# Performance work log

Measured on AMD Instinct MI355X. Metric: run time of the kernel, lower is better.

Reference implementation:

```python
import jax, jax.numpy as jnp
import numpy as np

BN_EPS = 1e-5


def _gin_layer(h, src, dst, w1, b1, w2, b2, gamma, beta):
    n = h.shape[0]
    # GINConv, eps=0: MLP(x + sum_{j->i} x_j); messages gathered at src, scattered to dst
    agg = jax.ops.segment_sum(h[src], dst, num_segments=n)
    h = agg + h
    h = jnp.maximum(h @ w1 + b1, 0.0) @ w2 + b2
    h = jnp.maximum(h, 0.0)  # F.relu after conv
    # BatchNorm1d, training-mode batch statistics (biased var)
    mean = h.mean(axis=0)
    var = h.var(axis=0)
    return (h - mean) * jax.lax.rsqrt(var + BN_EPS) * gamma + beta


def setup_inputs() -> dict:
    key = jax.random.key(0)
    ks = jax.random.split(key, 32)
    N, E, F_IN, DIM, L, G = 100000, 1600000, 128, 64, 3, 1000
    inp = {
        "x": jax.random.normal(ks[0], (N, F_IN), dtype=jnp.float32),
        "edge_index": jax.random.randint(ks[1], (2, E), 0, N, dtype=jnp.int64),
        "batch": jnp.sort(jax.random.randint(ks[2], (N,), 0, G, dtype=jnp.int64)),
        "num_graphs": G,
    }
    k = 3
    for i in range(L):
        din = F_IN if i == 0 else DIM
        inp[f"l{i}_w1"] = jax.random.normal(ks[k], (din, DIM), dtype=jnp.float32) * 0.05; k += 1
        inp[f"l{i}_b1"] = jnp.zeros((DIM,), dtype=jnp.float32)
        inp[f"l{i}_w2"] = jax.random.normal(ks[k], (DIM, DIM), dtype=jnp.float32) * 0.05; k += 1
        inp[f"l{i}_b2"] = jnp.zeros((DIM,), dtype=jnp.float32)
        inp[f"l{i}_gamma"] = jnp.ones((DIM,), dtype=jnp.float32)
        inp[f"l{i}_beta"] = jnp.zeros((DIM,), dtype=jnp.float32)
    return inp


def reference(x, edge_index, batch, num_graphs,
              l0_w1, l0_b1, l0_w2, l0_b2, l0_gamma, l0_beta,
              l1_w1, l1_b1, l1_w2, l1_b2, l1_gamma, l1_beta,
              l2_w1, l2_b1, l2_w2, l2_b2, l2_gamma, l2_beta):
    src, dst = edge_index[0], edge_index[1]
    params = [
        (l0_w1, l0_b1, l0_w2, l0_b2, l0_gamma, l0_beta),
        (l1_w1, l1_b1, l1_w2, l1_b2, l1_gamma, l1_beta),
        (l2_w1, l2_b1, l2_w2, l2_b2, l2_gamma, l2_beta),
    ]
    h = x
    xs = []
    for p in params:
        h = _gin_layer(h, src, dst, *p)
        xs.append(h)
    # global_add_pool per layer, then concat along features
    xpool = [jax.ops.segment_sum(h, batch, num_segments=num_graphs) for h in xs]
    return jnp.concatenate(xpool, axis=1), jnp.concatenate(xs, axis=1)
```

## Files before the change

### kernel.cpp

```cpp
#include <hip/hip_runtime.h>

#define DIM 64
#define XS_STRIDE 192
#define BN_EPS 1e-5f
#define B_MAX 512
#define P4_CAP 6144
#define CSR_CHUNK 16384
#define BSPACE 1280

__device__ inline unsigned pack_bf16x2(float lo, float hi) {
    unsigned ulo = __float_as_uint(lo); ulo = (ulo + 0x7FFFu + ((ulo >> 16) & 1u)) >> 16;
    unsigned uhi = __float_as_uint(hi); uhi = (uhi + 0x7FFFu + ((uhi >> 16) & 1u)) >> 16;
    return ulo | (uhi << 16);
}
__device__ inline float2 unpack_bf16x2(unsigned v) {
    return make_float2(__uint_as_float(v << 16), __uint_as_float(v & 0xFFFF0000u));
}

__global__ void setup_kernel(float* __restrict__ stats, unsigned* __restrict__ ybf, int N) {
    int t = threadIdx.x;
    if (t < 3 * 256) stats[t] = 0.f;
    if (t < 32) ybf[(size_t)N * 32 + t] = 0u;
}

__global__ __launch_bounds__(256) void p1_hist(const int* __restrict__ dsts, long long E,
                                               int NB1, int B, int* __restrict__ bh) {
    __shared__ int hist[B_MAX];
    const int i = blockIdx.x, t = threadIdx.x;
    for (int b = t; b < B; b += 256) hist[b] = 0;
    __syncthreads();
    long long s0 = (long long)i * CSR_CHUNK;
    long long s1 = s0 + CSR_CHUNK; if (s1 > E) s1 = E;
    for (long long e = s0 + t; e < s1; e += 256)
        atomicAdd(&hist[dsts[e] >> 8], 1);
    __syncthreads();
    for (int b = t; b < B; b += 256) bh[b * NB1 + i] = hist[b];
}

__global__ __launch_bounds__(1024) void p2_scan(int* __restrict__ bh, int total_n) {
    __shared__ int sbuf[2][1024];
    const int t = threadIdx.x;
    const int seg = (total_n + 1023) / 1024;
    int s0 = t * seg, s1 = s0 + seg; if (s1 > total_n) s1 = total_n;
    int s = 0;
    for (int i = s0; i < s1; i++) s += bh[i];
    sbuf[0][t] = s; __syncthreads();
    int c = 0;
    for (int o = 1; o < 1024; o <<= 1) {
        int val = sbuf[c][t];
        if (t >= o) val += sbuf[c][t - o];
        sbuf[c ^ 1][t] = val; __syncthreads(); c ^= 1;
    }
    int run = sbuf[c][t] - s;
    for (int i = s0; i < s1; i++) { int v = bh[i]; bh[i] = run; run += v; }
}

__global__ __launch_bounds__(256) void p3_part(const int* __restrict__ edges, long long E,
                                               int NB1, int B, const int* __restrict__ bh,
                                               unsigned* __restrict__ ebuf) {
    __shared__ int cur[B_MAX];
    const int i = blockIdx.x, t = threadIdx.x;
    for (int b = t; b < B; b += 256) cur[b] = bh[b * NB1 + i];
    __syncthreads();
    long long s0 = (long long)i * CSR_CHUNK;
    long long s1 = s0 + CSR_CHUNK; if (s1 > E) s1 = E;
    for (long long e = s0 + t; e < s1; e += 256) {
        int src = edges[e];
        int dst = edges[E + e];
        int b = dst >> 8;
        int pos = atomicAdd(&cur[b], 1);
        ebuf[pos] = (unsigned)src | ((unsigned)(dst & 255) << 24);
    }
}

__global__ __launch_bounds__(256) void p4_build(const unsigned* __restrict__ ebuf, long long E,
                                                int NB1, int B, const int* __restrict__ bh,
                                                int* __restrict__ offsets, int* __restrict__ psz,
                                                int* __restrict__ eidx, int N) {
    __shared__ unsigned lbuf[P4_CAP];
    __shared__ int hist[256];
    __shared__ int sbuf[2][256];
    __shared__ int cur[256];
    __shared__ int lstart[256];
    const int b = blockIdx.x, t = threadIdx.x;
    const int s = bh[b * NB1];
    const int e = (b + 1 < B) ? bh[(b + 1) * NB1] : (int)E;
    const int sz = e - s;
    const int ps = ((s + 3) & ~3) + b * BSPACE;
    const int next_raw = (b + 1 < B) ? bh[(b + 1) * NB1] : (int)E;
    const int next_ps = ((next_raw + 3) & ~3) + (b + 1) * BSPACE;
    const bool inl = (sz <= P4_CAP);
    if (inl) for (int k = t; k < sz; k += 256) lbuf[k] = ebuf[s + k];
    hist[t] = 0;
    __syncthreads();
    for (int k = t; k < sz; k += 256) {
        unsigned v = inl ? lbuf[k] : ebuf[s + k];
        atomicAdd(&hist[v >> 24], 1);
    }
    __syncthreads();
    const int deg = hist[t];
    const int pad = max(4, (deg + 3) & ~3);
    sbuf[0][t] = pad; __syncthreads();
    int c = 0;
    for (int o = 1; o < 256; o <<= 1) {
        int val = sbuf[c][t];
        if (t >= o) val += sbuf[c][t - o];
        sbuf[c ^ 1][t] = val; __syncthreads(); c ^= 1;
    }
    const int excl = sbuf[c][t] - pad;
    const int total = sbuf[c][255];
    const int node = b * 256 + t;
    if (node < N) { offsets[node] = ps + excl; psz[node] = pad; }
    lstart[t] = excl;
    cur[t] = 0;
    __syncthreads();
    for (int k = t; k < sz; k += 256) {
        unsigned v = inl ? lbuf[k] : ebuf[s + k];
        int dl = v >> 24;
        int pos = atomicAdd(&cur[dl], 1);
        eidx[ps + lstart[dl] + pos] = (int)(v & 0xFFFFFFu);
    }
    for (int k = deg; k < pad; k++) eidx[ps + excl + k] = N;
    __syncthreads();
    for (int i = ps + total + t; i < next_ps; i += 256) eidx[i] = N;
}

template<int DIN, bool FUSE>
__global__ __launch_bounds__(256) void proj_kernel(
    const float* __restrict__ h, int h_stride, int h_off,
    float* __restrict__ h_back,
    const float* __restrict__ w1,
    const float* __restrict__ scsh,
    unsigned* __restrict__ ybf, int N)
{
    constexpr int R = 32;
    __shared__ float w1s[DIN * DIM];
    __shared__ float hin[R][DIN];
    const int tid = threadIdx.x;
    const int row0 = blockIdx.x * R;

    for (int i = tid; i < DIN * DIM / 4; i += 256)
        *(float4*)&w1s[i * 4] = *(const float4*)&w1[i * 4];
    for (int i = tid; i < R * DIN / 4; i += 256) {
        int r = i / (DIN / 4), k4 = (i % (DIN / 4)) * 4;
        int row = row0 + r;
        float4 hv = make_float4(0.f, 0.f, 0.f, 0.f);
        if (row < N) {
            hv = *(const float4*)&h[(size_t)row * h_stride + h_off + k4];
            if (FUSE) {
                hv.x = hv.x * scsh[k4 + 0] + scsh[DIM + k4 + 0];
                hv.y = hv.y * scsh[k4 + 1] + scsh[DIM + k4 + 1];
                hv.z = hv.z * scsh[k4 + 2] + scsh[DIM + k4 + 2];
                hv.w = hv.w * scsh[k4 + 3] + scsh[DIM + k4 + 3];
                *(float4*)&h_back[(size_t)row * h_stride + h_off + k4] = hv;
            }
        }
        *(float4*)&hin[r][k4] = hv;
    }
    __syncthreads();

    const int hw = tid >> 5;
    const int hl = tid & 31;
    float a0[4], a1[4];
    #pragma unroll
    for (int q = 0; q < 4; q++) { a0[q] = 0.f; a1[q] = 0.f; }
    for (int k = 0; k < DIN; k++) {
        float w0 = w1s[k * DIM + 2 * hl];
        float w1v = w1s[k * DIM + 2 * hl + 1];
        #pragma unroll
        for (int q = 0; q < 4; q++) {
            float hv = hin[hw * 4 + q][k];
            a0[q] += hv * w0; a1[q] += hv * w1v;
        }
    }
    #pragma unroll
    for (int q = 0; q < 4; q++) {
        int row = row0 + hw * 4 + q;
        if (row < N) ybf[(size_t)row * 32 + hl] = pack_bf16x2(a0[q], a1[q]);
    }
}

__global__ __launch_bounds__(256) void aggmlp_kernel(
    const unsigned* __restrict__ ybf,
    const int* __restrict__ offsets, const int* __restrict__ psz,
    const int* __restrict__ eidx,
    const float* __restrict__ b1,
    const float* __restrict__ w2, const float* __restrict__ b2,
    float* __restrict__ xs, int xs_off,
    float* __restrict__ stats, int N)
{
    constexpr int R = 64;
    __shared__ float zin[R][DIM];
    __shared__ float sred[2][DIM];
    const int tid  = threadIdx.x;
    const int row0 = blockIdx.x * R;
    const int qw = tid >> 4;
    const int ql = tid & 15;
    const uint2* __restrict__ ybf2 = (const uint2*)ybf;

    if (tid < DIM) { sred[0][tid] = 0.f; sred[1][tid] = 0.f; }

    const float4 b1v = *(const float4*)&b1[ql * 4];
    int p0[4], sz[4];
    float ac[4][4];
    #pragma unroll
    for (int q = 0; q < 4; q++) {
        int node = row0 + qw * 4 + q;
        if (node < N) {
            p0[q] = offsets[node];
            sz[q] = psz[node];
            uint2 sv = ybf2[(size_t)node * 16 + ql];
            float2 lo = unpack_bf16x2(sv.x), hi = unpack_bf16x2(sv.y);
            ac[q][0] = lo.x + b1v.x; ac[q][1] = lo.y + b1v.y;
            ac[q][2] = hi.x + b1v.z; ac[q][3] = hi.y + b1v.w;
        } else {
            p0[q] = 0; sz[q] = 0;
            ac[q][0] = ac[q][1] = ac[q][2] = ac[q][3] = 0.f;
        }
    }
    int steps = 0;
    #pragma unroll
    for (int q = 0; q < 4; q++) steps = max(steps, sz[q] >> 2);

    for (int s = 0; s < steps; s++) {
        const int b4 = 4 * s;
        int4 e4[4];
        #pragma unroll
        for (int q = 0; q < 4; q++) {
            int off = max(0, min(b4, sz[q] - 4));
            e4[q] = *(const int4*)&eidx[p0[q] + off];
        }
        uint2 g[4][4];
        #pragma unroll
        for (int q = 0; q < 4; q++) {
            g[q][0] = ybf2[(size_t)e4[q].x * 16 + ql];
            g[q][1] = ybf2[(size_t)e4[q].y * 16 + ql];
            g[q][2] = ybf2[(size_t)e4[q].z * 16 + ql];
            g[q][3] = ybf2[(size_t)e4[q].w * 16 + ql];
        }
        #pragma unroll
        for (int q = 0; q < 4; q++) {
            const float m = (b4 < sz[q]) ? 1.f : 0.f;
            #pragma unroll
            for (int j = 0; j < 4; j++) {
                float2 lo = unpack_bf16x2(g[q][j].x), hi = unpack_bf16x2(g[q][j].y);
                ac[q][0] += lo.x * m; ac[q][1] += lo.y * m;
                ac[q][2] += hi.x * m; ac[q][3] += hi.y * m;
            }
        }
    }
    #pragma unroll
    for (int q = 0; q < 4; q++) {
        int r = qw * 4 + q;
        float4 z;
        z.x = fmaxf(ac[q][0], 0.f); z.y = fmaxf(ac[q][1], 0.f);
        z.z = fmaxf(ac[q][2], 0.f); z.w = fmaxf(ac[q][3], 0.f);
        *(float4*)&zin[r][ql * 4] = z;
    }
    __syncthreads();

    const int lane = tid & 63;
    const int wv_  = tid >> 6;
    float oacc[16];
    #pragma unroll
    for (int i = 0; i < 16; i++) oacc[i] = b2[lane];
    for (int k = 0; k < DIM; k++) {
        float w = w2[k * DIM + lane];
        #pragma unroll
        for (int i = 0; i < 16; i++) oacc[i] += zin[wv_ + 4 * i][k] * w;
    }
    float s1 = 0.f, s2 = 0.f;
    #pragma unroll
    for (int i = 0; i < 16; i++) {
        int row = row0 + wv_ + 4 * i;
        if (row < N) {
            float v = fmaxf(oacc[i], 0.f);
            xs[(size_t)row * XS_STRIDE + xs_off + lane] = v;
            s1 += v; s2 += v * v;
        }
    }
    atomicAdd(&sred[0][lane], s1);
    atomicAdd(&sred[1][lane], s2);
    __syncthreads();
    if (tid < DIM) {
        atomicAdd(&stats[tid], sred[0][tid]);
        atomicAdd(&stats[DIM + tid], sred[1][tid]);
    }
}

__global__ void bnparam_kernel(const float* __restrict__ stats,
                               const float* __restrict__ gamma, const float* __restrict__ beta,
                               float* __restrict__ sc, int N) {
    int c = threadIdx.x;
    float inv_n = 1.0f / (float)N;
    float mean = stats[c] * inv_n;
    float var  = stats[DIM + c] * inv_n - mean * mean;
    float scale = gamma[c] * rsqrtf(var + BN_EPS);
    sc[c] = scale;
    sc[DIM + c] = beta[c] - mean * scale;
}

__global__ void pool_kernel(float* __restrict__ xs, const int* __restrict__ batch,
                            float* __restrict__ pool, const float* __restrict__ scsh2, int N) {
    int g = blockIdx.x;
    int tid = threadIdx.x;
    int lo = 0, hi = N;
    while (lo < hi) { int mid = (lo + hi) >> 1; if (batch[mid] < g) lo = mid + 1; else hi = mid; }
    int start = lo;
    hi = N;
    while (lo < hi) { int mid = (lo + hi) >> 1; if (batch[mid] < g + 1) lo = mid + 1; else hi = mid; }
    int end = lo;
    float s = 0.f;
    if (tid < 2 * DIM) {
        for (int n = start; n < end; n++) s += xs[(size_t)n * XS_STRIDE + tid];
    } else {
        const float sc = scsh2[tid - 2 * DIM];
        const float sh = scsh2[DIM + tid - 2 * DIM];
        for (int n = start; n < end; n++) {
            size_t p = (size_t)n * XS_STRIDE + tid;
            float v = xs[p] * sc + sh;
            xs[p] = v;
            s += v;
        }
    }
    pool[(size_t)g * XS_STRIDE + tid] = s;
}

extern "C" void kernel_launch(void* const* d_in, const int* in_sizes, int n_in,
                              void* d_out, int out_size, void* d_ws, size_t ws_size,
                              hipStream_t stream) {
    const float* x     = (const float*)d_in[0];
    const int*   edges = (const int*)d_in[1];
    const int*   batch = (const int*)d_in[2];

    const int  N    = in_sizes[2];
    const long long E = in_sizes[1] / 2;
    const int  F_IN = in_sizes[0] / N;
    const int  G    = out_size / XS_STRIDE - N;

    const float* W[3][6];
    for (int l = 0; l < 3; l++)
        for (int p = 0; p < 6; p++)
            W[l][p] = (const float*)d_in[4 + l * 6 + p];

    float* out_pool = (float*)d_out;
    float* out_xs   = out_pool + (size_t)G * XS_STRIDE;

    const int B   = (N + 255) >> 8;
    const int NB1 = (int)((E + CSR_CHUNK - 1) / CSR_CHUNK);
    const int EPAD = (int)(((E + 3) & ~3LL) + (long long)B * BSPACE + 64);

    unsigned* ybf  = (unsigned*)d_ws;
    float* stats   = (float*)(ybf + (size_t)(N + 1) * 32);
    int*   offsets = (int*)(stats + 3 * 256);
    int*   psz     = offsets + N + 1;
    int*   eidx    = psz + N;
    unsigned* ebuf = (unsigned*)(eidx + EPAD);
    int*   bh      = (int*)(ebuf + E);

    const int pblocks = (N + 31) / 32;
    const int ablocks = (N + 63) / 64;

    setup_kernel<<<1, 1024, 0, stream>>>(stats, ybf, N);
    p1_hist<<<NB1, 256, 0, stream>>>(edges + E, E, NB1, B, bh);
    p2_scan<<<1, 1024, 0, stream>>>(bh, B * NB1);
    p3_part<<<NB1, 256, 0, stream>>>(edges, E, NB1, B, bh, ebuf);
    p4_build<<<B, 256, 0, stream>>>(ebuf, E, NB1, B, bh, offsets, psz, eidx, N);

    for (int l = 0; l < 3; l++) {
        const int h_off = (l == 0) ? 0 : (l - 1) * DIM;
        float* statsL = stats + l * 256;

        if (l == 0)
            proj_kernel<128, false><<<pblocks, 256, 0, stream>>>(
                x, F_IN, 0, nullptr, W[l][0], nullptr, ybf, N);
        else
            proj_kernel<64, true><<<pblocks, 256, 0, stream>>>(
                out_xs, XS_STRIDE, h_off, out_xs,
                W[l][0], stats + (l - 1) * 256 + 2 * DIM, ybf, N);

        aggmlp_kernel<<<ablocks, 256, 0, stream>>>(ybf, offsets, psz, eidx,
            W[l][1], W[l][2], W[l][3], out_xs, l * DIM, statsL, N);

        bnparam_kernel<<<1, 64, 0, stream>>>(statsL, W[l][4], W[l][5], statsL + 2 * DIM, N);
    }

    pool_kernel<<<G, XS_STRIDE, 0, stream>>>(out_xs, batch, out_pool,
                                             stats + 2 * 256 + 2 * DIM, N);
}
```

Before: 453.3 us.

## Sort nodes by degree within 64-node groups to balance aggregation work

During CSR construction, each group of 64 nodes is ranked by in-degree and a permutation array is written. The aggregation+MLP kernel then processes nodes in that permuted order, so the 4 nodes handled by each 16-lane group have similar degrees and the step count (the max over those nodes) wastes fewer iterations. The cost is an extra indirection load per node, scattered row writes to the output, and a 64-iteration rank loop in the build kernel.

After: 460.9 us. Within noise of the previous version (+1.7%).

```diff
diff --git a/kernel.cpp b/kernel.cpp
--- a/kernel.cpp
+++ b/kernel.cpp
@@ -76,7 +76,8 @@
 __global__ __launch_bounds__(256) void p4_build(const unsigned* __restrict__ ebuf, long long E,
                                                 int NB1, int B, const int* __restrict__ bh,
                                                 int* __restrict__ offsets, int* __restrict__ psz,
-                                                int* __restrict__ eidx, int N) {
+                                                int* __restrict__ eidx, int* __restrict__ perm,
+                                                int N) {
     __shared__ unsigned lbuf[P4_CAP];
     __shared__ int hist[256];
     __shared__ int sbuf[2][256];
@@ -100,6 +101,16 @@
     __syncthreads();
     const int deg = hist[t];
     const int pad = max(4, (deg + 3) & ~3);
+    {
+        const int grp = t >> 6, lt = t & 63;
+        int rank = 0;
+        #pragma unroll 8
+        for (int i = 0; i < 64; i++) {
+            int od = hist[grp * 64 + i];
+            rank += (od < deg) || (od == deg && i < lt);
+        }
+        perm[b * 256 + grp * 64 + rank] = b * 256 + t;
+    }
     sbuf[0][t] = pad; __syncthreads();
     int c = 0;
     for (int o = 1; o < 256; o <<= 1) {
@@ -183,7 +194,7 @@
 __global__ __launch_bounds__(256) void aggmlp_kernel(
     const unsigned* __restrict__ ybf,
     const int* __restrict__ offsets, const int* __restrict__ psz,
-    const int* __restrict__ eidx,
+    const int* __restrict__ eidx, const int* __restrict__ perm,
     const float* __restrict__ b1,
     const float* __restrict__ w2, const float* __restrict__ b2,
     float* __restrict__ xs, int xs_off,
@@ -205,7 +216,7 @@
     float ac[4][4];
     #pragma unroll
     for (int q = 0; q < 4; q++) {
-        int node = row0 + qw * 4 + q;
+        int node = perm[row0 + qw * 4 + q];
         if (node < N) {
             p0[q] = offsets[node];
             sz[q] = psz[node];
@@ -272,10 +283,10 @@
     float s1 = 0.f, s2 = 0.f;
     #pragma unroll
     for (int i = 0; i < 16; i++) {
-        int row = row0 + wv_ + 4 * i;
-        if (row < N) {
+        int node = perm[row0 + wv_ + 4 * i];
+        if (node < N) {
             float v = fmaxf(oacc[i], 0.f);
-            xs[(size_t)row * XS_STRIDE + xs_off + lane] = v;
+            xs[(size_t)node * XS_STRIDE + xs_off + lane] = v;
             s1 += v; s2 += v * v;
         }
     }
@@ -354,7 +365,8 @@
     float* stats   = (float*)(ybf + (size_t)(N + 1) * 32);
     int*   offsets = (int*)(stats + 3 * 256);
     int*   psz     = offsets + N + 1;
-    int*   eidx    = psz + N;
+    int*   perm    = psz + N;
+    int*   eidx    = perm + B * 256;
     unsigned* ebuf = (unsigned*)(eidx + EPAD);
     int*   bh      = (int*)(ebuf + E);
 
@@ -365,7 +377,7 @@
     p1_hist<<<NB1, 256, 0, stream>>>(edges + E, E, NB1, B, bh);
     p2_scan<<<1, 1024, 0, stream>>>(bh, B * NB1);
     p3_part<<<NB1, 256, 0, stream>>>(edges, E, NB1, B, bh, ebuf);
-    p4_build<<<B, 256, 0, stream>>>(ebuf, E, NB1, B, bh, offsets, psz, eidx, N);
+    p4_build<<<B, 256, 0, stream>>>(ebuf, E, NB1, B, bh, offsets, psz, eidx, perm, N);
 
     for (int l = 0; l < 3; l++) {
         const int h_off = (l == 0) ? 0 : (l - 1) * DIM;
@@ -379,7 +391,7 @@
                 out_xs, XS_STRIDE, h_off, out_xs,
                 W[l][0], stats + (l - 1) * 256 + 2 * DIM, ybf, N);
 
-        aggmlp_kernel<<<ablocks, 256, 0, stream>>>(ybf, offsets, psz, eidx,
+        aggmlp_kernel<<<ablocks, 256, 0, stream>>>(ybf, offsets, psz, eidx, perm,
             W[l][1], W[l][2], W[l][3], out_xs, l * DIM, statsL, N);
 
         bnparam_kernel<<<1, 64, 0, stream>>>(statsL, W[l][4], W[l][5], statsL + 2 * DIM, N);
```
